# Performance work log

Measured on AMD Instinct MI355X. Metric: run time of the kernel, lower is better.

The kernel has to match this reference:

```python
import jax, jax.numpy as jnp
import numpy as np

B, S, H = 4, 512, 768
D, M = 24, 96          # hdim_proj_dim, hdim_mlp_hidden
O = 2 * max(128, H // 2)  # val_mlp hidden = 768


def setup_inputs() -> dict:
    key = jax.random.key(0)
    ks = jax.random.split(key, 14)
    u = lambda k, shp, fan_in: jax.random.uniform(k, shp, jnp.float32, -1.0, 1.0) / np.float32(np.sqrt(fan_in))
    return {
        'H_j': jax.random.normal(ks[0], (B, S, H), jnp.float32),
        'H_i': jax.random.normal(ks[1], (B, S, H), jnp.float32),
        'Wpj': u(ks[2], (H, D), H),
        'Wpi': u(ks[3], (H, D), H),
        'Ws1': u(ks[4], (4 * D, M), 4 * D),
        'bs1': u(ks[5], (M,), 4 * D),
        'ws2': u(ks[6], (M,), M),
        'bs2': u(ks[7], (), M),
        'Wv1': u(ks[8], (3 * H, O), 3 * H),
        'bv1': u(ks[9], (O,), 3 * H),
        'Wv2': u(ks[10], (O, H), O),
        'bv2': u(ks[11], (H,), O),
        'alpha': jnp.float32(0.05),
        'attn_mask': jnp.ones((B, S), jnp.int32),
    }


def reference(H_j, H_i, Wpj, Wpi, Ws1, bs1, ws2, bs2, Wv1, bv1, Wv2, bv2, alpha, attn_mask):
    # Projections [B,S,D]
    Zj = H_j @ Wpj
    Zi = H_i @ Wpi
    # 4term score MLP, first layer decomposed over the concat blocks:
    # cat(Zj_p, Zi_p, Zj_p*Zi_p, |Zj_p - Zi_p|) @ Ws1
    W1j, W1i, W1h, W1d = Ws1[:D], Ws1[D:2 * D], Ws1[2 * D:3 * D], Ws1[3 * D:]
    tj = Zj @ W1j                                   # [B,P,M]
    ti = Zi @ W1i                                   # [B,Q,M]
    th = jnp.einsum('bpd,bqd,dm->bpqm', Zj, Zi, W1h)  # hadamard term
    diff = jnp.abs(Zj[:, :, None, :] - Zi[:, None, :, :])  # [B,P,Q,D]
    td = jnp.einsum('bpqd,dm->bpqm', diff, W1d)
    hid = jax.nn.relu(tj[:, :, None, :] + ti[:, None, :, :] + th + td + bs1)  # [B,P,Q,M]
    logits = jnp.einsum('bpqm,m->bpq', hid, ws2) + bs2  # [B,P,Q]
    # mask over source tokens (last dim); token_temp == 1.0 so no division
    mask = attn_mask.astype(logits.dtype)
    logits = logits + (1.0 - mask)[:, None, :] * jnp.finfo(logits.dtype).min
    probs = jax.nn.softmax(logits, axis=-1)
    ctx = jnp.einsum('bpq,bqh->bph', probs, H_i)    # [B,S,H]
    # val_mlp on cat(ctx, H_j, ctx*H_j), first layer decomposed
    Wc, Wj, Wh = Wv1[:H], Wv1[H:2 * H], Wv1[2 * H:]
    mhid = jax.nn.relu(ctx @ Wc + H_j @ Wj + (ctx * H_j) @ Wh + bv1)
    msg = mhid @ Wv2 + bv2
    # dropout is identity in eval mode
    return alpha * msg
```

## Files before the change

### kernel.cpp

```cpp
#include <hip/hip_runtime.h>
#include <hip/hip_bf16.h>

#define Bb 4
#define Ss 512
#define Hh 768
#define Dd 24
#define Mm 96
#define Oo 768

typedef __bf16 bf16x8 __attribute__((ext_vector_type(8)));
typedef float f32x4 __attribute__((ext_vector_type(4)));

__global__ __launch_bounds__(256) void proj_kernel(
    const float* __restrict__ Hj, const float* __restrict__ Hi,
    const float* __restrict__ Wpj, const float* __restrict__ Wpi,
    float* __restrict__ Zj, float* __restrict__ Zi)
{
    const int row = blockIdx.x;
    const int which = blockIdx.y;
    const float* src = (which ? Hi : Hj) + (size_t)row * Hh;
    const float* W = which ? Wpi : Wpj;
    float* Z = which ? Zi : Zj;
    __shared__ float rowbuf[Hh];
    __shared__ float partial[8][Dd];
    const int tid = threadIdx.x;
    for (int i = tid; i < Hh; i += 256) rowbuf[i] = src[i];
    __syncthreads();
    if (tid < 192) {
        const int d = tid % Dd;
        const int c = tid / Dd;
        const int h0 = c * 96;
        float s = 0.f;
        #pragma unroll 4
        for (int h = h0; h < h0 + 96; ++h) s = fmaf(rowbuf[h], W[h * Dd + d], s);
        partial[c][d] = s;
    }
    __syncthreads();
    if (tid < Dd) {
        float s = 0.f;
        #pragma unroll
        for (int c = 0; c < 8; ++c) s += partial[c][tid];
        Z[(size_t)row * Dd + tid] = s;
    }
}

__global__ __launch_bounds__(256) void transpose_bf16_kernel(
    const float* __restrict__ src, __bf16* __restrict__ dst,
    int R, int C, long sbatch, long dbatch)
{
    const float* s = src + (size_t)blockIdx.z * sbatch;
    __bf16* d = dst + (size_t)blockIdx.z * dbatch;
    __shared__ float t[32][33];
    const int x = threadIdx.x & 31, y = threadIdx.x >> 5;
    const int c0 = blockIdx.x * 32, r0 = blockIdx.y * 32;
    #pragma unroll
    for (int i = 0; i < 4; ++i)
        t[y + 8 * i][x] = s[(size_t)(r0 + y + 8 * i) * C + c0 + x];
    __syncthreads();
    #pragma unroll
    for (int i = 0; i < 4; ++i)
        d[(size_t)(c0 + y + 8 * i) * R + r0 + x] = (__bf16)t[x][y + 8 * i];
}

__global__ __launch_bounds__(256) void hjconv_kernel(
    const float* __restrict__ Hjf, __bf16* __restrict__ Ac)
{
    const int idx = blockIdx.x * 256 + threadIdx.x;
    const int row = idx / 96, c8 = idx % 96;
    const float* s = Hjf + (size_t)row * Hh + c8 * 8;
    const float4 u = *(const float4*)s;
    const float4 v = *(const float4*)(s + 4);
    bf16x8 o;
    o[0]=(__bf16)u.x; o[1]=(__bf16)u.y; o[2]=(__bf16)u.z; o[3]=(__bf16)u.w;
    o[4]=(__bf16)v.x; o[5]=(__bf16)v.y; o[6]=(__bf16)v.z; o[7]=(__bf16)v.w;
    *(bf16x8*)&Ac[(size_t)row * 2304 + Hh + c8 * 8] = o;
}

__global__ __launch_bounds__(256) void pair_kernel(
    const float* __restrict__ Zj, const float* __restrict__ Zi,
    const float* __restrict__ Ws1, const float* __restrict__ bs1,
    const float* __restrict__ ws2, const float* __restrict__ bs2p,
    const int* __restrict__ mask, __bf16* __restrict__ probs)
{
    const int bp = blockIdx.x;
    const int b  = bp >> 9;
    const int tid  = threadIdx.x;
    const int lane = tid & 63;
    const int wid  = tid >> 6;
    const int col  = lane & 15;
    const int g    = lane >> 4;

    __shared__ float zjall[Dd];
    __shared__ float rowadd[Mm];
    __shared__ float logitsl[Ss];
    __shared__ float red[8];

    if (tid < Dd) zjall[tid] = Zj[(size_t)bp * Dd + tid];
    __syncthreads();
    if (tid < Mm) {
        float s = bs1[tid];
        #pragma unroll
        for (int d = 0; d < Dd; ++d) s = fmaf(zjall[d], Ws1[d * Mm + tid], s);
        rowadd[tid] = s;
    }
    __syncthreads();

    float zj8[8];
    if (g < 3) {
        const float* zr = Zj + (size_t)bp * Dd + g * 8;
        const float4 u = *(const float4*)zr;
        const float4 v = *(const float4*)(zr + 4);
        zj8[0]=u.x; zj8[1]=u.y; zj8[2]=u.z; zj8[3]=u.w;
        zj8[4]=v.x; zj8[5]=v.y; zj8[6]=v.z; zj8[7]=v.w;
    } else {
        #pragma unroll
        for (int j = 0; j < 8; ++j) zj8[j] = 0.f;
    }

    bf16x8 bw[6][2];
    float ws2r[6];
    #pragma unroll
    for (int n = 0; n < 6; ++n) {
        const int m = n * 16 + col;
        ws2r[n] = ws2[m];
        bf16x8 b0, b1;
        if (g < 3) {
            #pragma unroll
            for (int j = 0; j < 8; ++j) {
                const int d = g * 8 + j;
                b0[j] = (__bf16)(fmaf(zj8[j], Ws1[(2 * Dd + d) * Mm + m],
                                      Ws1[(Dd + d) * Mm + m]));
                b1[j] = (__bf16)(Ws1[(3 * Dd + d) * Mm + m]);
            }
        } else {
            #pragma unroll
            for (int j = 0; j < 8; ++j) { b0[j] = (__bf16)0.f; b1[j] = (__bf16)0.f; }
            b0[0] = (__bf16)rowadd[m];
        }
        bw[n][0] = b0; bw[n][1] = b1;
    }

    const float* zib = Zi + (size_t)b * Ss * Dd;

    #pragma unroll 2
    for (int t = 0; t < 8; ++t) {
        const int q0 = wid * 128 + t * 16;
        bf16x8 a0, a1;
        if (g < 3) {
            const float* zr = zib + (size_t)(q0 + col) * Dd + g * 8;
            const float4 u = *(const float4*)zr;
            const float4 v = *(const float4*)(zr + 4);
            a0[0]=(__bf16)u.x; a0[1]=(__bf16)u.y; a0[2]=(__bf16)u.z; a0[3]=(__bf16)u.w;
            a0[4]=(__bf16)v.x; a0[5]=(__bf16)v.y; a0[6]=(__bf16)v.z; a0[7]=(__bf16)v.w;
            a1[0]=(__bf16)fabsf(zj8[0]-u.x); a1[1]=(__bf16)fabsf(zj8[1]-u.y);
            a1[2]=(__bf16)fabsf(zj8[2]-u.z); a1[3]=(__bf16)fabsf(zj8[3]-u.w);
            a1[4]=(__bf16)fabsf(zj8[4]-v.x); a1[5]=(__bf16)fabsf(zj8[5]-v.y);
            a1[6]=(__bf16)fabsf(zj8[6]-v.z); a1[7]=(__bf16)fabsf(zj8[7]-v.w);
        } else {
            #pragma unroll
            for (int j = 0; j < 8; ++j) { a0[j] = (__bf16)0.f; a1[j] = (__bf16)0.f; }
            a0[0] = (__bf16)1.0f;
        }

        f32x4 acc[6];
        #pragma unroll
        for (int n = 0; n < 6; ++n) acc[n] = (f32x4){0.f, 0.f, 0.f, 0.f};
        #pragma unroll
        for (int n = 0; n < 6; ++n) {
            acc[n] = __builtin_amdgcn_mfma_f32_16x16x32_bf16(a0, bw[n][0], acc[n], 0, 0, 0);
            acc[n] = __builtin_amdgcn_mfma_f32_16x16x32_bf16(a1, bw[n][1], acc[n], 0, 0, 0);
        }

        float lsum[4] = {0.f, 0.f, 0.f, 0.f};
        #pragma unroll
        for (int n = 0; n < 6; ++n)
            #pragma unroll
            for (int r = 0; r < 4; ++r)
                lsum[r] = fmaf(fmaxf(acc[n][r], 0.f), ws2r[n], lsum[r]);
        #pragma unroll
        for (int off = 1; off <= 8; off <<= 1) {
            #pragma unroll
            for (int r = 0; r < 4; ++r) lsum[r] += __shfl_xor(lsum[r], off);
        }
        if (col == 0) {
            float4 o = {lsum[0], lsum[1], lsum[2], lsum[3]};
            *(float4*)&logitsl[q0 + g * 4] = o;
        }
    }
    __syncthreads();

    const float bs2v = bs2p[0];
    const int* mrow = mask + (size_t)b * Ss;
    float l0 = logitsl[tid]       + bs2v + (1.0f - (float)mrow[tid])       * (-3.402823466e+38f);
    float l1 = logitsl[tid + 256] + bs2v + (1.0f - (float)mrow[tid + 256]) * (-3.402823466e+38f);
    float vmax = fmaxf(l0, l1);
    #pragma unroll
    for (int off = 32; off > 0; off >>= 1) vmax = fmaxf(vmax, __shfl_xor(vmax, off));
    if (lane == 0) red[wid] = vmax;
    __syncthreads();
    const float mx = fmaxf(fmaxf(red[0], red[1]), fmaxf(red[2], red[3]));
    const float e0 = __expf(l0 - mx);
    const float e1 = __expf(l1 - mx);
    float vs = e0 + e1;
    #pragma unroll
    for (int off = 32; off > 0; off >>= 1) vs += __shfl_xor(vs, off);
    if (lane == 0) red[4 + wid] = vs;
    __syncthreads();
    const float inv = 1.0f / (red[4] + red[5] + red[6] + red[7]);
    __bf16* prow = probs + (size_t)bp * Ss;
    prow[tid] = (__bf16)(e0 * inv);
    prow[tid + 256] = (__bf16)(e1 * inv);
}

template<int MODE>
__global__ __launch_bounds__(256) void gemm_kernel(
    const __bf16* __restrict__ A, const __bf16* __restrict__ Bt,
    const float* __restrict__ Hjf, const float* __restrict__ bias,
    const float* __restrict__ alphap,
    __bf16* __restrict__ obf, float* __restrict__ of)
{
    constexpr int K = (MODE == 0) ? 512 : (MODE == 1) ? 2304 : 768;
    constexpr int NIT = K / 64;
    constexpr int LDT = 72;

    __shared__ __bf16 As[64 * LDT];
    __shared__ __bf16 Bs[64 * LDT];

    const int tid = threadIdx.x;
    const int lane = tid & 63;
    const int wid = tid >> 6;
    const int col = lane & 15, g = lane >> 4;
    const int wm = wid >> 1, wn = wid & 1;
    const int r0 = blockIdx.x * 64;
    const int n0 = blockIdx.y * 64;
    const __bf16* Btb = (MODE == 0) ? Bt + (size_t)(r0 >> 9) * (Hh * Ss) : Bt;

    const int srow = tid >> 2;
    const int sc8  = (tid & 3) * 16;
    const __bf16* ag = A   + (size_t)(r0 + srow) * K + sc8;
    const __bf16* bg = Btb + (size_t)(n0 + srow) * K + sc8;
    __bf16* asl = &As[srow * LDT + sc8];
    __bf16* bsl = &Bs[srow * LDT + sc8];

    bf16x8 ra0 = *(const bf16x8*)(ag);
    bf16x8 ra1 = *(const bf16x8*)(ag + 8);
    bf16x8 rb0 = *(const bf16x8*)(bg);
    bf16x8 rb1 = *(const bf16x8*)(bg + 8);

    f32x4 acc[2][2];
    #pragma unroll
    for (int mi = 0; mi < 2; ++mi)
        #pragma unroll
        for (int ni = 0; ni < 2; ++ni) acc[mi][ni] = (f32x4){0.f, 0.f, 0.f, 0.f};

    for (int it = 0; it < NIT; ++it) {
        __syncthreads();
        *(bf16x8*)(asl)     = ra0;
        *(bf16x8*)(asl + 8) = ra1;
        *(bf16x8*)(bsl)     = rb0;
        *(bf16x8*)(bsl + 8) = rb1;
        __syncthreads();
        if (it + 1 < NIT) {
            const int kk = (it + 1) * 64;
            ra0 = *(const bf16x8*)(ag + kk);
            ra1 = *(const bf16x8*)(ag + kk + 8);
            rb0 = *(const bf16x8*)(bg + kk);
            rb1 = *(const bf16x8*)(bg + kk + 8);
        }
        #pragma unroll
        for (int h = 0; h < 2; ++h) {
            bf16x8 a0 = *(const bf16x8*)&As[(wm * 32 + col)      * LDT + h * 32 + g * 8];
            bf16x8 a1 = *(const bf16x8*)&As[(wm * 32 + 16 + col) * LDT + h * 32 + g * 8];
            bf16x8 b0 = *(const bf16x8*)&Bs[(wn * 32 + col)      * LDT + h * 32 + g * 8];
            bf16x8 b1 = *(const bf16x8*)&Bs[(wn * 32 + 16 + col) * LDT + h * 32 + g * 8];
            acc[0][0] = __builtin_amdgcn_mfma_f32_16x16x32_bf16(a0, b0, acc[0][0], 0, 0, 0);
            acc[0][1] = __builtin_amdgcn_mfma_f32_16x16x32_bf16(a0, b1, acc[0][1], 0, 0, 0);
            acc[1][0] = __builtin_amdgcn_mfma_f32_16x16x32_bf16(a1, b0, acc[1][0], 0, 0, 0);
            acc[1][1] = __builtin_amdgcn_mfma_f32_16x16x32_bf16(a1, b1, acc[1][1], 0, 0, 0);
        }
    }

    const float al = (MODE == 2) ? alphap[0] : 0.f;
    #pragma unroll
    for (int mi = 0; mi < 2; ++mi) {
        #pragma unroll
        for (int r = 0; r < 4; ++r) {
            const int row = r0 + wm * 32 + mi * 16 + g * 4 + r;
            #pragma unroll
            for (int ni = 0; ni < 2; ++ni) {
                const int cn = n0 + wn * 32 + ni * 16 + col;
                const float v = acc[mi][ni][r];
                if (MODE == 0) {
                    const float hjv = Hjf[(size_t)row * Hh + cn];
                    obf[(size_t)row * 2304 + cn] = (__bf16)v;
                    obf[(size_t)row * 2304 + 1536 + cn] = (__bf16)(v * hjv);
                } else if (MODE == 1) {
                    obf[(size_t)row * Oo + cn] = (__bf16)fmaxf(v + bias[cn], 0.f);
                } else {
                    of[(size_t)row * Hh + cn] = al * (v + bias[cn]);
                }
            }
        }
    }
}

extern "C" void kernel_launch(void* const* d_in, const int* in_sizes, int n_in,
                              void* d_out, int out_size, void* d_ws, size_t ws_size,
                              hipStream_t stream)
{
    const float* Hj  = (const float*)d_in[0];
    const float* Hi  = (const float*)d_in[1];
    const float* Wpj = (const float*)d_in[2];
    const float* Wpi = (const float*)d_in[3];
    const float* Ws1 = (const float*)d_in[4];
    const float* bs1 = (const float*)d_in[5];
    const float* ws2 = (const float*)d_in[6];
    const float* bs2 = (const float*)d_in[7];
    const float* Wv1 = (const float*)d_in[8];
    const float* bv1 = (const float*)d_in[9];
    const float* Wv2 = (const float*)d_in[10];
    const float* bv2 = (const float*)d_in[11];
    const float* alpha = (const float*)d_in[12];
    const int* mask  = (const int*)d_in[13];

    float* ws = (float*)d_ws;
    float* Zj = ws;
    float* Zi = Zj + 49152;
    float* R0f = Zi + 49152;
    float* R1f = R0f + 524288;
    float* Acat_f = R1f + 786432;
    float* Wv1T_f = Acat_f + 2359296;

    __bf16* probs_bf = (__bf16*)R0f;
    __bf16* Wv2T     = (__bf16*)R0f;
    __bf16* HiT      = (__bf16*)R1f;
    __bf16* mhid_bf  = (__bf16*)R1f;
    __bf16* Acat     = (__bf16*)Acat_f;
    __bf16* Wv1T     = (__bf16*)Wv1T_f;

    proj_kernel<<<dim3(Bb * Ss, 2), 256, 0, stream>>>(Hj, Hi, Wpj, Wpi, Zj, Zi);
    transpose_bf16_kernel<<<dim3(Hh / 32, Ss / 32, Bb), 256, 0, stream>>>(
        Hi, HiT, Ss, Hh, (long)Ss * Hh, (long)Hh * Ss);
    transpose_bf16_kernel<<<dim3(Oo / 32, 3 * Hh / 32, 1), 256, 0, stream>>>(
        Wv1, Wv1T, 3 * Hh, Oo, 0, 0);
    hjconv_kernel<<<dim3(768), 256, 0, stream>>>(Hj, Acat);
    pair_kernel<<<dim3(Bb * Ss), 256, 0, stream>>>(Zj, Zi, Ws1, bs1, ws2, bs2, mask, probs_bf);
    gemm_kernel<0><<<dim3(2048 / 64, Hh / 64), 256, 0, stream>>>(
        probs_bf, HiT, Hj, nullptr, nullptr, Acat, nullptr);
    transpose_bf16_kernel<<<dim3(Hh / 32, Oo / 32, 1), 256, 0, stream>>>(
        Wv2, Wv2T, Oo, Hh, 0, 0);
    gemm_kernel<1><<<dim3(2048 / 64, Oo / 64), 256, 0, stream>>>(
        Acat, Wv1T, nullptr, bv1, nullptr, mhid_bf, nullptr);
    gemm_kernel<2><<<dim3(2048 / 64, Hh / 64), 256, 0, stream>>>(
        mhid_bf, Wv2T, nullptr, bv2, alpha, nullptr, (float*)d_out);
}
```

Before: 190.2 us.

## Precompute per-row bf16 score weights in separate kernel and swap MFMA operands

Adds a wprep kernel that computes, for each query row p, the combined bf16 first-layer weight tiles (Zj-scaled hadamard plus Zi weights, the row bias term, and the diff weights). These are stored in a workspace buffer. pair_kernel now loads these tiles directly instead of rebuilding them from fp32 Ws1 in every block, and swaps the MFMA A/B operands so the per-q vectors are the B operand. That lets the reduction over M use two cross-row shuffles instead of four-step 16-lane butterflies, and it also prefetches the next Zi tile. The cost is an extra kernel launch and roughly 25MB of extra global writes and reads for the Bw buffer.

```diff
diff --git a/kernel.cpp b/kernel.cpp
--- a/kernel.cpp
+++ b/kernel.cpp
@@ -76,11 +76,49 @@
     *(bf16x8*)&Ac[(size_t)row * 2304 + Hh + c8 * 8] = o;
 }
 
+__global__ __launch_bounds__(256) void wprep_kernel(
+    const float* __restrict__ Zj, const float* __restrict__ Ws1,
+    const float* __restrict__ bs1, __bf16* __restrict__ Bw)
+{
+    __shared__ float W[96][97];
+    const int tid = threadIdx.x;
+    for (int i = tid; i < 96 * 96; i += 256)
+        W[i / 96][i % 96] = Ws1[i];
+    __syncthreads();
+    const int m = tid;
+    if (m >= 96) return;
+    const float bs1m = bs1[m];
+    for (int pp = 0; pp < 8; ++pp) {
+        const int p = blockIdx.x * 8 + pp;
+        const float* zr = Zj + (size_t)p * Dd;
+        float tj = bs1m;
+        #pragma unroll
+        for (int d = 0; d < Dd; ++d) tj = fmaf(zr[d], W[d][m], tj);
+        bf16x8 o[8];
+        #pragma unroll
+        for (int i = 0; i < 8; ++i) {
+            #pragma unroll
+            for (int j = 0; j < 8; ++j) {
+                const int k = i * 8 + j;
+                float v;
+                if (k < 24)                 v = fmaf(zr[k], W[48 + k][m], W[24 + k][m]);
+                else if (k == 24)           v = tj;
+                else if (k >= 32 && k < 56) v = W[72 + (k - 32)][m];
+                else                        v = 0.f;
+                o[i][j] = (__bf16)v;
+            }
+        }
+        __bf16* dst = Bw + (((size_t)p * 96 + m) << 6);
+        #pragma unroll
+        for (int i = 0; i < 8; ++i) *(bf16x8*)(dst + i * 8) = o[i];
+    }
+}
+
 __global__ __launch_bounds__(256) void pair_kernel(
     const float* __restrict__ Zj, const float* __restrict__ Zi,
-    const float* __restrict__ Ws1, const float* __restrict__ bs1,
-    const float* __restrict__ ws2, const float* __restrict__ bs2p,
-    const int* __restrict__ mask, __bf16* __restrict__ probs)
+    const __bf16* __restrict__ Bw, const float* __restrict__ ws2,
+    const float* __restrict__ bs2p, const int* __restrict__ mask,
+    __bf16* __restrict__ probs)
 {
     const int bp = blockIdx.x;
     const int b  = bp >> 9;
@@ -90,20 +128,22 @@
     const int col  = lane & 15;
     const int g    = lane >> 4;
 
-    __shared__ float zjall[Dd];
-    __shared__ float rowadd[Mm];
     __shared__ float logitsl[Ss];
     __shared__ float red[8];
 
-    if (tid < Dd) zjall[tid] = Zj[(size_t)bp * Dd + tid];
-    __syncthreads();
-    if (tid < Mm) {
-        float s = bs1[tid];
-        #pragma unroll
-        for (int d = 0; d < Dd; ++d) s = fmaf(zjall[d], Ws1[d * Mm + tid], s);
-        rowadd[tid] = s;
-    }
-    __syncthreads();
+    bf16x8 aw[6][2];
+    #pragma unroll
+    for (int n = 0; n < 6; ++n) {
+        const __bf16* base = Bw + (((size_t)bp * 96 + n * 16 + col) << 6) + g * 8;
+        aw[n][0] = *(const bf16x8*)(base);
+        aw[n][1] = *(const bf16x8*)(base + 32);
+    }
+    float ws2r[6][4];
+    #pragma unroll
+    for (int n = 0; n < 6; ++n) {
+        const float4 w4 = *(const float4*)&ws2[n * 16 + g * 4];
+        ws2r[n][0] = w4.x; ws2r[n][1] = w4.y; ws2r[n][2] = w4.z; ws2r[n][3] = w4.w;
+    }
 
     float zj8[8];
     if (g < 3) {
@@ -117,49 +157,33 @@
         for (int j = 0; j < 8; ++j) zj8[j] = 0.f;
     }
 
-    bf16x8 bw[6][2];
-    float ws2r[6];
-    #pragma unroll
-    for (int n = 0; n < 6; ++n) {
-        const int m = n * 16 + col;
-        ws2r[n] = ws2[m];
+    const float* zib = Zi + (size_t)b * Ss * Dd;
+    const int ko = (g < 3) ? g * 8 : 0;
+
+    float4 cu, cv;
+    {
+        const float* zr = zib + (size_t)(wid * 128 + col) * Dd + ko;
+        cu = *(const float4*)zr; cv = *(const float4*)(zr + 4);
+    }
+
+    for (int t = 0; t < 8; ++t) {
+        const float4 u = cu, v = cv;
+        if (t + 1 < 8) {
+            const float* zr = zib + (size_t)(wid * 128 + (t + 1) * 16 + col) * Dd + ko;
+            cu = *(const float4*)zr; cv = *(const float4*)(zr + 4);
+        }
         bf16x8 b0, b1;
         if (g < 3) {
-            #pragma unroll
-            for (int j = 0; j < 8; ++j) {
-                const int d = g * 8 + j;
-                b0[j] = (__bf16)(fmaf(zj8[j], Ws1[(2 * Dd + d) * Mm + m],
-                                      Ws1[(Dd + d) * Mm + m]));
-                b1[j] = (__bf16)(Ws1[(3 * Dd + d) * Mm + m]);
-            }
+            b0[0]=(__bf16)u.x; b0[1]=(__bf16)u.y; b0[2]=(__bf16)u.z; b0[3]=(__bf16)u.w;
+            b0[4]=(__bf16)v.x; b0[5]=(__bf16)v.y; b0[6]=(__bf16)v.z; b0[7]=(__bf16)v.w;
+            b1[0]=(__bf16)fabsf(zj8[0]-u.x); b1[1]=(__bf16)fabsf(zj8[1]-u.y);
+            b1[2]=(__bf16)fabsf(zj8[2]-u.z); b1[3]=(__bf16)fabsf(zj8[3]-u.w);
+            b1[4]=(__bf16)fabsf(zj8[4]-v.x); b1[5]=(__bf16)fabsf(zj8[5]-v.y);
+            b1[6]=(__bf16)fabsf(zj8[6]-v.z); b1[7]=(__bf16)fabsf(zj8[7]-v.w);
         } else {
             #pragma unroll
             for (int j = 0; j < 8; ++j) { b0[j] = (__bf16)0.f; b1[j] = (__bf16)0.f; }
-            b0[0] = (__bf16)rowadd[m];
-        }
-        bw[n][0] = b0; bw[n][1] = b1;
-    }
-
-    const float* zib = Zi + (size_t)b * Ss * Dd;
-
-    #pragma unroll 2
-    for (int t = 0; t < 8; ++t) {
-        const int q0 = wid * 128 + t * 16;
-        bf16x8 a0, a1;
-        if (g < 3) {
-            const float* zr = zib + (size_t)(q0 + col) * Dd + g * 8;
-            const float4 u = *(const float4*)zr;
-            const float4 v = *(const float4*)(zr + 4);
-            a0[0]=(__bf16)u.x; a0[1]=(__bf16)u.y; a0[2]=(__bf16)u.z; a0[3]=(__bf16)u.w;
-            a0[4]=(__bf16)v.x; a0[5]=(__bf16)v.y; a0[6]=(__bf16)v.z; a0[7]=(__bf16)v.w;
-            a1[0]=(__bf16)fabsf(zj8[0]-u.x); a1[1]=(__bf16)fabsf(zj8[1]-u.y);
-            a1[2]=(__bf16)fabsf(zj8[2]-u.z); a1[3]=(__bf16)fabsf(zj8[3]-u.w);
-            a1[4]=(__bf16)fabsf(zj8[4]-v.x); a1[5]=(__bf16)fabsf(zj8[5]-v.y);
-            a1[6]=(__bf16)fabsf(zj8[6]-v.z); a1[7]=(__bf16)fabsf(zj8[7]-v.w);
-        } else {
-            #pragma unroll
-            for (int j = 0; j < 8; ++j) { a0[j] = (__bf16)0.f; a1[j] = (__bf16)0.f; }
-            a0[0] = (__bf16)1.0f;
+            b0[0] = (__bf16)1.0f;
         }
 
         f32x4 acc[6];
@@ -167,25 +191,19 @@
         for (int n = 0; n < 6; ++n) acc[n] = (f32x4){0.f, 0.f, 0.f, 0.f};
         #pragma unroll
         for (int n = 0; n < 6; ++n) {
-            acc[n] = __builtin_amdgcn_mfma_f32_16x16x32_bf16(a0, bw[n][0], acc[n], 0, 0, 0);
-            acc[n] = __builtin_amdgcn_mfma_f32_16x16x32_bf16(a1, bw[n][1], acc[n], 0, 0, 0);
-        }
-
-        float lsum[4] = {0.f, 0.f, 0.f, 0.f};
+            acc[n] = __builtin_amdgcn_mfma_f32_16x16x32_bf16(aw[n][0], b0, acc[n], 0, 0, 0);
+            acc[n] = __builtin_amdgcn_mfma_f32_16x16x32_bf16(aw[n][1], b1, acc[n], 0, 0, 0);
+        }
+
+        float lsum = 0.f;
         #pragma unroll
         for (int n = 0; n < 6; ++n)
             #pragma unroll
             for (int r = 0; r < 4; ++r)
-                lsum[r] = fmaf(fmaxf(acc[n][r], 0.f), ws2r[n], lsum[r]);
-        #pragma unroll
-        for (int off = 1; off <= 8; off <<= 1) {
-            #pragma unroll
-            for (int r = 0; r < 4; ++r) lsum[r] += __shfl_xor(lsum[r], off);
-        }
-        if (col == 0) {
-            float4 o = {lsum[0], lsum[1], lsum[2], lsum[3]};
-            *(float4*)&logitsl[q0 + g * 4] = o;
-        }
+                lsum = fmaf(fmaxf(acc[n][r], 0.f), ws2r[n][r], lsum);
+        lsum += __shfl_xor(lsum, 16);
+        lsum += __shfl_xor(lsum, 32);
+        if (lane < 16) logitsl[wid * 128 + t * 16 + lane] = lsum;
     }
     __syncthreads();
 
@@ -330,6 +348,7 @@
     float* R1f = R0f + 524288;
     float* Acat_f = R1f + 786432;
     float* Wv1T_f = Acat_f + 2359296;
+    float* Bw_f   = Wv1T_f + 884736;
 
     __bf16* probs_bf = (__bf16*)R0f;
     __bf16* Wv2T     = (__bf16*)R0f;
@@ -337,14 +356,16 @@
     __bf16* mhid_bf  = (__bf16*)R1f;
     __bf16* Acat     = (__bf16*)Acat_f;
     __bf16* Wv1T     = (__bf16*)Wv1T_f;
+    __bf16* Bw       = (__bf16*)Bw_f;
 
     proj_kernel<<<dim3(Bb * Ss, 2), 256, 0, stream>>>(Hj, Hi, Wpj, Wpi, Zj, Zi);
+    wprep_kernel<<<dim3(256), 256, 0, stream>>>(Zj, Ws1, bs1, Bw);
     transpose_bf16_kernel<<<dim3(Hh / 32, Ss / 32, Bb), 256, 0, stream>>>(
         Hi, HiT, Ss, Hh, (long)Ss * Hh, (long)Hh * Ss);
     transpose_bf16_kernel<<<dim3(Oo / 32, 3 * Hh / 32, 1), 256, 0, stream>>>(
         Wv1, Wv1T, 3 * Hh, Oo, 0, 0);
     hjconv_kernel<<<dim3(768), 256, 0, stream>>>(Hj, Acat);
-    pair_kernel<<<dim3(Bb * Ss), 256, 0, stream>>>(Zj, Zi, Ws1, bs1, ws2, bs2, mask, probs_bf);
+    pair_kernel<<<dim3(Bb * Ss), 256, 0, stream>>>(Zj, Zi, Bw, ws2, bs2, mask, probs_bf);
     gemm_kernel<0><<<dim3(2048 / 64, Hh / 64), 256, 0, stream>>>(
         probs_bf, HiT, Hj, nullptr, nullptr, Acat, nullptr);
     transpose_bf16_kernel<<<dim3(Hh / 32, Oo / 32, 1), 256, 0, stream>>>(
```

Result: slower. 207.1 us (+8.9%).
